# Kernel optimization log

Measured on AMD Instinct MI355X. Metric: run time of the kernel, lower is better.

Reference implementation:

```python
import jax, jax.numpy as jnp
import numpy as np


def _segsum(v, idx, n):
    return jax.ops.segment_sum(v, idx, num_segments=n)


def _rdl(z, n_dst, Wna, We, Wi, es, ed, is_, id_):
    """Relationship_Decoupled_layer: node softmax attn + per-edge attn.
    e-channel (mode etype): softmax over 2 logits; i-channel: sigmoid(1 logit)."""
    zd = z[:n_dst]
    node_alpha = jax.nn.softmax(zd @ Wna, axis=1)                      # [nd,2]
    e_e = jax.nn.softmax(jnp.concatenate([z[es], zd[ed]], axis=-1) @ We, axis=1)  # [Ee,2]
    e_i = jax.nn.sigmoid(jnp.concatenate([z[is_], zd[id_]], axis=-1) @ Wi)        # [Ei,1]
    return node_alpha, e_e, e_i


def _one_agg(z, n_dst, W, b, na, e_e, es, ed):
    """One_Neighbor_Aggregation: mean over nbrs of e[:,0]*Linear(z_src), relu, + alpha0*z_dst.
    Linear is applied on src nodes once (linearity) instead of per-edge."""
    zd = na[:, 0:1] * z[:n_dst]
    wz = z @ W + b                                                     # [n_src,D]
    s = _segsum(e_e[:, 0:1] * wz[es], ed, n_dst)                       # [nd,D]
    deg = _segsum(jnp.ones((es.shape[0], 1), z.dtype), ed, n_dst)
    f = jax.nn.relu(s / jnp.maximum(deg, 1.0))
    return f + zd


def _nia(z, n_dst, na, e_e, es, ed, e_i, is_, id_):
    """Neighbor_Interaction_Aggregation: e_h (mode etype, attn col 1) and i_h
    (other etype, sigmoid attn), cross term via polarization identity, + alpha1*z_dst."""
    zd = na[:, 1:2] * z[:n_dst]
    e_h = _segsum(e_e[:, 1:2] * z[es], ed, n_dst)
    i_h = _segsum(e_i * z[is_], id_, n_dst)
    inter = jax.nn.relu(0.5 * (jnp.square(e_h + i_h) - jnp.square(e_h) - jnp.square(i_h)))
    return inter + zd


def setup_inputs() -> dict:
    key = jax.random.key(0)
    ks = jax.random.split(key, 32)
    F, D, O = 256, 128, 64
    n_src0, n_dst0, E0 = 100000, 25000, 500000
    n_src1, n_dst1, E1 = 25000, 5000, 100000

    def ri(k, n, hi):
        return jax.random.randint(k, (n,), 0, hi, dtype=jnp.int32)

    inp = {
        'feat': jax.random.normal(ks[0], (n_src0, F), jnp.float32),
        'src0_cor': ri(ks[1], E0, n_src0), 'dst0_cor': ri(ks[2], E0, n_dst0),
        'src0_sim': ri(ks[3], E0, n_src0), 'dst0_sim': ri(ks[4], E0, n_dst0),
        'src1_cor': ri(ks[5], E1, n_src1), 'dst1_cor': ri(ks[6], E1, n_dst1),
        'src1_sim': ri(ks[7], E1, n_src1), 'dst1_sim': ri(ks[8], E1, n_dst1),
        'n_dst0': n_dst0, 'n_dst1': n_dst1,
    }
    s = 0.05  # keep attention logits / activations in a sane range
    inp['Win'] = jax.random.normal(ks[9], (2, F, D)) * s
    inp['b_in'] = jnp.zeros((2, D), jnp.float32)
    inp['na1'] = jax.random.normal(ks[10], (2, D, 2)) * s
    inp['ea1'] = jax.random.normal(ks[11], (2, 2 * D, 2)) * s
    inp['ia1'] = jax.random.normal(ks[12], (2, 2 * D, 1)) * s
    inp['W1'] = jax.random.normal(ks[13], (2, D, D)) * s
    inp['b1'] = jnp.zeros((2, D), jnp.float32)
    inp['na2'] = jax.random.normal(ks[14], (2, D, 2)) * s
    inp['ea2'] = jax.random.normal(ks[15], (2, 2 * D, 2)) * s
    inp['ia2'] = jax.random.normal(ks[16], (2, 2 * D, 1)) * s
    inp['W2'] = jax.random.normal(ks[17], (2, D, D)) * s
    inp['b2'] = jnp.zeros((2, D), jnp.float32)
    inp['Wout'] = jax.random.normal(ks[18], (2, D, O)) * s
    inp['bout'] = jnp.zeros((2, O), jnp.float32)
    return inp


def reference(feat, src0_cor, dst0_cor, src0_sim, dst0_sim,
              src1_cor, dst1_cor, src1_sim, dst1_sim, n_dst0, n_dst1,
              Win, b_in, na1, ea1, ia1, W1, b1, na2, ea2, ia2, W2, b2, Wout, bout):
    # mode index 0 = 'cor', 1 = 'sim'; e-channel = mode etype, i-channel = other etype
    blk0 = {0: (src0_cor, dst0_cor, src0_sim, dst0_sim),
            1: (src0_sim, dst0_sim, src0_cor, dst0_cor)}
    blk1 = {0: (src1_cor, dst1_cor, src1_sim, dst1_sim),
            1: (src1_sim, dst1_sim, src1_cor, dst1_cor)}
    outs = []
    for m in range(2):
        es0, ed0, is0, id0 = blk0[m]
        es1, ed1, is1, id1 = blk1[m]
        z = feat @ Win[m] + b_in[m]                                    # fc_input (eval: dropout = identity)
        # layer 1 on block0
        na, ee, ei = _rdl(z, n_dst0, na1[m], ea1[m], ia1[m], es0, ed0, is0, id0)
        one = _one_agg(z, n_dst0, W1[m], b1[m], na, ee, es0, ed0)
        nia = _nia(z, n_dst0, na, ee, es0, ed0, ei, is0, id0)
        z = 0.5 * (one + nia)                                          # [n_dst0, D]
        # layer 2 on block1
        na, ee, ei = _rdl(z, n_dst1, na2[m], ea2[m], ia2[m], es1, ed1, is1, id1)
        one = _one_agg(z, n_dst1, W2[m], b2[m], na, ee, es1, ed1)
        nia = _nia(z, n_dst1, na, ee, es1, ed1, ei, is1, id1)
        z = 0.5 * (one + nia)                                          # [n_dst1, D]
        outs.append(z @ Wout[m] + bout[m])
    return jnp.stack(outs)                                             # [2, n_dst1, O] (cor, sim)
```

## Files before the change

kernel.cpp:

```cpp
#include <hip/hip_runtime.h>
#include <hip/hip_bf16.h>
#include <math.h>

#define F_DIM 256
#define D_DIM 128
#define O_DIM 64
#define NS0   100000
#define ND0   25000
#define E0_N  500000
#define NS1   25000
#define ND1   5000
#define E1_N  100000

#define NBE0  1954
#define NBE1  391
#define NB_CSR (2 * NBE0 + 2 * NBE1)
#define NB_WPREP 576

typedef __attribute__((ext_vector_type(8))) short s8v;
typedef __attribute__((ext_vector_type(4))) float f4v;

struct CPtr4 { const int *p0, *p1, *p2, *p3; };
struct MPtr4 { int *p0, *p1, *p2, *p3; };

__device__ __forceinline__ float2 unpack2(uint u) {
    union { uint i; float f; } a, b;
    a.i = (u & 0xffffu) << 16; b.i = u & 0xffff0000u;
    return make_float2(a.f, b.f);
}
__device__ __forceinline__ ushort f2bf(float f) {
    __hip_bfloat16 h = __float2bfloat16(f);
    return *(ushort*)&h;
}
__device__ __forceinline__ float u2f(uint u) {
    union { uint i; float f; } v; v.i = u; return v.f;
}
__device__ __forceinline__ uint f2u(float f) {
    union { uint i; float f; } v; v.f = f; return v.i;
}

__global__ __launch_bounds__(256) void gemm_l0(
    const float* __restrict__ A,
    const ushort* __restrict__ Btb,
    const float* __restrict__ biasb,
    ushort* __restrict__ Coutb, size_t coutstr, int M)
{
    constexpr int PA = 40;
    __shared__ ushort As[64 * PA];
    __shared__ ushort Bs[2][128 * PA];

    const int tid = threadIdx.x;
    const int row0 = blockIdx.x * 64;
    const int wave = tid >> 6, lane = tid & 63;
    const int l15 = lane & 15, l4 = lane >> 4;
    const int wm0 = (wave >> 1) * 32;
    const int wn0 = (wave & 1) * 64;

    f4v acc[2][2][4];
    #pragma unroll
    for (int m2 = 0; m2 < 2; ++m2)
        #pragma unroll
        for (int i = 0; i < 2; ++i)
            #pragma unroll
            for (int j = 0; j < 4; ++j)
                acc[m2][i][j] = (f4v)(0.0f);

    for (int kc = 0; kc < F_DIM; kc += 32) {
        __syncthreads();
        {
            int r = tid >> 2, g = (tid & 3) * 8;
            int gr = row0 + r;
            float4 v0 = make_float4(0.f, 0.f, 0.f, 0.f);
            float4 v1 = make_float4(0.f, 0.f, 0.f, 0.f);
            if (gr < M) {
                v0 = *(const float4*)(A + (size_t)gr * F_DIM + kc + g);
                v1 = *(const float4*)(A + (size_t)gr * F_DIM + kc + g + 4);
            }
            ushort4 o0, o1;
            o0.x = f2bf(v0.x); o0.y = f2bf(v0.y); o0.z = f2bf(v0.z); o0.w = f2bf(v0.w);
            o1.x = f2bf(v1.x); o1.y = f2bf(v1.y); o1.z = f2bf(v1.z); o1.w = f2bf(v1.w);
            *(ushort4*)(&As[r * PA + g]) = o0;
            *(ushort4*)(&As[r * PA + g + 4]) = o1;
        }
        #pragma unroll
        for (int m2 = 0; m2 < 2; ++m2)
            #pragma unroll
            for (int it = 0; it < 2; ++it) {
                int f = tid + it * 256;
                int r = f >> 2, g = (f & 3) * 8;
                *(float4*)(&Bs[m2][r * PA + g]) =
                    *(const float4*)(Btb + m2 * (D_DIM * F_DIM) + (size_t)r * F_DIM + kc + g);
            }
        __syncthreads();

        s8v af[2];
        #pragma unroll
        for (int i = 0; i < 2; ++i)
            af[i] = *(const s8v*)(&As[(wm0 + i * 16 + l15) * PA + l4 * 8]);
        #pragma unroll
        for (int m2 = 0; m2 < 2; ++m2) {
            s8v bfr[4];
            #pragma unroll
            for (int j = 0; j < 4; ++j)
                bfr[j] = *(const s8v*)(&Bs[m2][(wn0 + j * 16 + l15) * PA + l4 * 8]);
            #pragma unroll
            for (int i = 0; i < 2; ++i)
                #pragma unroll
                for (int j = 0; j < 4; ++j)
                    acc[m2][i][j] = __builtin_amdgcn_mfma_f32_16x16x32_bf16(
                        af[i], bfr[j], acc[m2][i][j], 0, 0, 0);
        }
    }

    #pragma unroll
    for (int m2 = 0; m2 < 2; ++m2)
        #pragma unroll
        for (int i = 0; i < 2; ++i)
            #pragma unroll
            for (int ii = 0; ii < 4; ++ii) {
                int row = row0 + wm0 + i * 16 + l4 * 4 + ii;
                if (row < M) {
                    #pragma unroll
                    for (int j = 0; j < 4; ++j) {
                        int col = wn0 + j * 16 + l15;
                        Coutb[m2 * coutstr + (size_t)row * D_DIM + col] =
                            f2bf(acc[m2][i][j][ii] + biasb[m2 * D_DIM + col]);
                    }
                }
            }
}

template<int NW, int KD, int EPI>
__global__ __launch_bounds__(256) void mfma_gemm(
    const ushort* __restrict__ Ab, size_t astr,
    const ushort* __restrict__ Btb, size_t btstr,
    const float* __restrict__ biasb, size_t bstr,
    const float* __restrict__ cvecb, size_t cvstr,
    const float* __restrict__ partialb, size_t pstr,
    void* __restrict__ Coutb, size_t coutstr, int M)
{
    const int m = blockIdx.y;
    const ushort* A = Ab + m * astr;
    const ushort* Bt = Btb + m * btstr;
    const float* bias = biasb + m * bstr;
    const float* cvec = (EPI == 2) ? cvecb + m * cvstr : nullptr;
    const float* partial = (EPI == 2) ? partialb + m * pstr : nullptr;
    char* Cout = (char*)Coutb + m * coutstr * (EPI == 1 ? 4 : 2);

    constexpr int PA = 40;
    constexpr int WAVES_M = (NW == 128) ? 2 : 4;
    constexpr int WM = 128 / WAVES_M;
    constexpr int TM = WM / 16;
    constexpr int TN = 4;
    __shared__ ushort As[128 * PA];
    __shared__ ushort Bs[NW * PA];

    const int tid  = threadIdx.x;
    const int row0 = blockIdx.x * 128;
    const int wave = tid >> 6, lane = tid & 63;
    const int l15 = lane & 15, l4 = lane >> 4;
    int wm0, wn0;
    if (NW == 128) { wm0 = (wave >> 1) * 64; wn0 = (wave & 1) * 64; }
    else           { wm0 = wave * WM;        wn0 = 0; }

    f4v acc[TM][TN];
    #pragma unroll
    for (int i = 0; i < TM; ++i)
        #pragma unroll
        for (int j = 0; j < TN; ++j)
            acc[i][j] = (f4v)(0.0f);

    for (int kc = 0; kc < KD; kc += 32) {
        __syncthreads();
        #pragma unroll
        for (int it = 0; it < 2; ++it) {
            int f = tid + it * 256;
            int r = f >> 2, g = (f & 3) * 8;
            int gr = row0 + r;
            float4 v = make_float4(0.f, 0.f, 0.f, 0.f);
            if (gr < M) v = *(const float4*)(A + (size_t)gr * KD + kc + g);
            *(float4*)(&As[r * PA + g]) = v;
        }
        #pragma unroll
        for (int it = 0; it < NW * 32 / (256 * 8); ++it) {
            int f = tid + it * 256;
            int r = f >> 2, g = (f & 3) * 8;
            *(float4*)(&Bs[r * PA + g]) = *(const float4*)(Bt + (size_t)r * KD + kc + g);
        }
        __syncthreads();

        s8v af[TM], bfr[TN];
        #pragma unroll
        for (int i = 0; i < TM; ++i)
            af[i] = *(const s8v*)(&As[(wm0 + i * 16 + l15) * PA + l4 * 8]);
        #pragma unroll
        for (int j = 0; j < TN; ++j)
            bfr[j] = *(const s8v*)(&Bs[(wn0 + j * 16 + l15) * PA + l4 * 8]);
        #pragma unroll
        for (int i = 0; i < TM; ++i)
            #pragma unroll
            for (int j = 0; j < TN; ++j)
                acc[i][j] = __builtin_amdgcn_mfma_f32_16x16x32_bf16(
                    af[i], bfr[j], acc[i][j], 0, 0, 0);
    }

    #pragma unroll
    for (int i = 0; i < TM; ++i) {
        #pragma unroll
        for (int ii = 0; ii < 4; ++ii) {
            int row = row0 + wm0 + i * 16 + l4 * 4 + ii;
            if (row < M) {
                #pragma unroll
                for (int j = 0; j < TN; ++j) {
                    int col = wn0 + j * 16 + l15;
                    float a = acc[i][j][ii];
                    if (EPI == 1) {
                        ((float*)Cout)[(size_t)row * NW + col] = a + bias[col];
                    } else {
                        float val = a + cvec[row] * bias[col];
                        float o = partial[(size_t)row * NW + col] + 0.5f * fmaxf(val, 0.f);
                        ((ushort*)Cout)[(size_t)row * NW + col] = f2bf(o);
                    }
                }
            }
        }
    }
}

__global__ void histo4_prep(CPtr4 ed, MPtr4 cnt,
    const float* __restrict__ Win, const float* __restrict__ W1,
    const float* __restrict__ W2,  const float* __restrict__ Wout,
    ushort* __restrict__ Wtin, ushort* __restrict__ Wt1,
    ushort* __restrict__ Wt2,  ushort* __restrict__ Wtout)
{
    int b = blockIdx.x, t = threadIdx.x;
    if (b >= NB_CSR) {
        int i = (b - NB_CSR) * 256 + t;
        if (i < 65536) {
            int m = i >> 15, r = i & 32767, k = r >> 7, n = r & 127;
            Wtin[m * 32768 + n * 256 + k] = f2bf(Win[m * 32768 + k * 128 + n]);
        } else if (i < 98304) {
            int i2 = i - 65536;
            int m = i2 >> 14, r = i2 & 16383, k = r >> 7, n = r & 127;
            Wt1[m * 16384 + n * 128 + k] = f2bf(W1[m * 16384 + k * 128 + n]);
        } else if (i < 131072) {
            int i2 = i - 98304;
            int m = i2 >> 14, r = i2 & 16383, k = r >> 7, n = r & 127;
            Wt2[m * 16384 + n * 128 + k] = f2bf(W2[m * 16384 + k * 128 + n]);
        } else if (i < 147456) {
            int i2 = i - 131072;
            int m = i2 >> 13, r = i2 & 8191, k = r >> 6, n = r & 63;
            Wtout[m * 8192 + n * 128 + k] = f2bf(Wout[m * 8192 + k * 64 + n]);
        }
        return;
    }
    const int* edp; int* cp; int e, E;
    if (b < NBE0)          { edp = ed.p0; cp = cnt.p0; e = b * 256 + t;              E = E0_N; }
    else if (b < 2 * NBE0) { edp = ed.p1; cp = cnt.p1; e = (b - NBE0) * 256 + t;     E = E0_N; }
    else if (b < 2 * NBE0 + NBE1)
                           { edp = ed.p2; cp = cnt.p2; e = (b - 2 * NBE0) * 256 + t; E = E1_N; }
    else                   { edp = ed.p3; cp = cnt.p3; e = (b - 2 * NBE0 - NBE1) * 256 + t; E = E1_N; }
    if (e < E) atomicAdd(&cp[edp[e]], 1);
}

__global__ __launch_bounds__(1024) void exscan4(MPtr4 cnt, MPtr4 row, MPtr4 head)
{
    __shared__ int part[1024];
    const int b = blockIdx.x, t = threadIdx.x;
    int* cp; int* rp; int* hp; int n;
    if (b == 0)      { cp = cnt.p0; rp = row.p0; hp = head.p0; n = ND0; }
    else if (b == 1) { cp = cnt.p1; rp = row.p1; hp = head.p1; n = ND0; }
    else if (b == 2) { cp = cnt.p2; rp = row.p2; hp = head.p2; n = ND1; }
    else             { cp = cnt.p3; rp = row.p3; hp = head.p3; n = ND1; }

    const int chunk = (n + 1023) >> 10;
    const int start = t * chunk;
    int s = 0;
    for (int i = 0; i < chunk; ++i) {
        int idx = start + i;
        if (idx < n) s += cp[idx];
    }
    part[t] = s;
    __syncthreads();
    for (int off = 1; off < 1024; off <<= 1) {
        int v = (t >= off) ? part[t - off] : 0;
        __syncthreads();
        part[t] += v;
        __syncthreads();
    }
    int run = (t == 0) ? 0 : part[t - 1];
    for (int i = 0; i < chunk; ++i) {
        int idx = start + i;
        if (idx < n) { rp[idx] = run; hp[idx] = run; run += cp[idx]; }
    }
    if (t == 1023) rp[n] = part[1023];
}

__global__ void build4(CPtr4 es, CPtr4 ed, MPtr4 head, MPtr4 src)
{
    int b = blockIdx.x, t = threadIdx.x;
    const int *esp, *edp; int *hp, *sp; int e, E;
    if (b < NBE0)          { esp = es.p0; edp = ed.p0; hp = head.p0; sp = src.p0; e = b * 256 + t;              E = E0_N; }
    else if (b < 2 * NBE0) { esp = es.p1; edp = ed.p1; hp = head.p1; sp = src.p1; e = (b - NBE0) * 256 + t;     E = E0_N; }
    else if (b < 2 * NBE0 + NBE1)
                           { esp = es.p2; edp = ed.p2; hp = head.p2; sp = src.p2; e = (b - 2 * NBE0) * 256 + t; E = E1_N; }
    else                   { esp = es.p3; edp = ed.p3; hp = head.p3; sp = src.p3; e = (b - 2 * NBE0 - NBE1) * 256 + t; E = E1_N; }
    if (e >= E) return;
    int p = atomicAdd(&hp[edp[e]], 1);
    sp[p] = esp[e];
}

#define NP_NPB 128
__global__ __launch_bounds__(256) void node_proj(
    const ushort* __restrict__ zb, size_t zstr,
    const float* __restrict__ Web, const float* __restrict__ Wib,
    float* __restrict__ psb, float* __restrict__ qsb,
    float* __restrict__ pdb, float* __restrict__ qdb,
    int n_src, int n_dst)
{
    const int m = blockIdx.y;
    const ushort* z = zb + m * zstr;
    const float* We = Web + m * 512;
    const float* Wi = Wib + m * 256;
    float* ps = psb + (size_t)m * NS0 * 2;
    float* qs = qsb + (size_t)m * NS0;
    float* pd = pdb + (size_t)m * ND0 * 2;
    float* qd = qdb + (size_t)m * ND0;

    __shared__ float w[6][D_DIM];
    for (int k = threadIdx.x; k < D_DIM; k += 256) {
        w[0][k] = We[k * 2 + 0];
        w[1][k] = We[k * 2 + 1];
        w[2][k] = Wi[k];
        w[3][k] = We[(D_DIM + k) * 2 + 0];
        w[4][k] = We[(D_DIM + k) * 2 + 1];
        w[5][k] = Wi[D_DIM + k];
    }
    __syncthreads();

    const int sub = threadIdx.x & 7;
    const int g   = threadIdx.x >> 3;

    float wr[6][16];
    #pragma unroll
    for (int c = 0; c < 6; ++c)
        #pragma unroll
        for (int q = 0; q < 4; ++q) {
            float4 f = *(const float4*)(&w[c][sub * 16 + q * 4]);
            wr[c][q * 4 + 0] = f.x; wr[c][q * 4 + 1] = f.y;
            wr[c][q * 4 + 2] = f.z; wr[c][q * 4 + 3] = f.w;
        }

    #pragma unroll
    for (int it = 0; it < 4; ++it) {
        int node = blockIdx.x * NP_NPB + it * 32 + g;
        if (node >= n_src) continue;
        const ushort* zp = z + (size_t)node * D_DIM + sub * 16;
        uint4 ra = *(const uint4*)zp;
        uint4 rb = *(const uint4*)(zp + 8);
        uint rr[8] = {ra.x, ra.y, ra.z, ra.w, rb.x, rb.y, rb.z, rb.w};
        float p[6] = {0.f, 0.f, 0.f, 0.f, 0.f, 0.f};
        #pragma unroll
        for (int e = 0; e < 8; ++e) {
            float2 f2 = unpack2(rr[e]);
            #pragma unroll
            for (int c = 0; c < 6; ++c)
                p[c] += f2.x * wr[c][2 * e] + f2.y * wr[c][2 * e + 1];
        }
        #pragma unroll
        for (int off = 4; off > 0; off >>= 1)
            #pragma unroll
            for (int c = 0; c < 6; ++c)
                p[c] += __shfl_down(p[c], off);

        if (sub == 0) {
            *(float2*)(ps + (size_t)node * 2) = make_float2(p[0], p[1]);
            qs[node] = p[2];
            if (node < n_dst) {
                *(float2*)(pd + (size_t)node * 2) = make_float2(p[3], p[4]);
                qd[node] = p[5];
            }
        }
    }
}

__global__ __launch_bounds__(256) void edge_att(
    const float* __restrict__ psb, const float* __restrict__ pdb,
    const float* __restrict__ qsb, const float* __restrict__ qdb,
    const int* __restrict__ row_c, const int* __restrict__ src_c,
    const int* __restrict__ row_s, const int* __restrict__ src_s,
    uint2* __restrict__ epkb, uint2* __restrict__ ipkb,
    float* __restrict__ cvecb, int n_dst)
{
    const int m = blockIdx.y;
    const int d = blockIdx.x * 4 + (threadIdx.x >> 6);
    const int lane = threadIdx.x & 63;
    if (d >= n_dst) return;

    const float* ps = psb + (size_t)m * NS0 * 2;
    const float* qs = qsb + (size_t)m * NS0;
    const float* pdv = pdb + (size_t)m * ND0 * 2;
    const float* qdv = qdb + (size_t)m * ND0;
    const int* erow = m ? row_s : row_c;
    const int* esrc = m ? src_s : src_c;
    const int* irow = m ? row_c : row_s;
    const int* isrc = m ? src_c : src_s;
    uint2* epk = epkb + (size_t)m * E0_N;
    uint2* ipk = ipkb + (size_t)m * E0_N;
    float* cvec = cvecb + (size_t)m * ND0;

    const float pd0 = pdv[2 * d], pd1 = pdv[2 * d + 1];
    const float qdd = qdv[d];

    const int b0 = erow[d], b1 = erow[d + 1];
    float se0 = 0.f;
    for (int j = b0 + lane; j < b1; j += 64) {
        int s = esrc[j];
        float2 pp = *(const float2*)(ps + 2 * (size_t)s);
        float l0 = pp.x + pd0, l1 = pp.y + pd1;
        float mx = fmaxf(l0, l1);
        float x0 = __expf(l0 - mx), x1 = __expf(l1 - mx);
        float e0 = x0 / (x0 + x1);
        epk[j] = make_uint2(f2u(e0), (uint)s);
        se0 += e0;
    }
    #pragma unroll
    for (int off = 32; off > 0; off >>= 1)
        se0 += __shfl_down(se0, off);
    if (lane == 0) cvec[d] = se0 / fmaxf((float)(b1 - b0), 1.0f);

    const int c0 = irow[d], c1 = irow[d + 1];
    for (int j = c0 + lane; j < c1; j += 64) {
        int s = isrc[j];
        float q = qs[s] + qdd;
        float sg = 1.0f / (1.0f + __expf(-q));
        ipk[j] = make_uint2(f2u(sg), (uint)s);
    }
}

__global__ __launch_bounds__(256) void gather_acc(
    const ushort* __restrict__ zb, size_t zstr,
    const uint2* __restrict__ epkb, const uint2* __restrict__ ipkb,
    const int* __restrict__ row_c, const int* __restrict__ row_s,
    ushort* __restrict__ h0base, float* __restrict__ partialb, int n_dst)
{
    const int m = blockIdx.y;
    const int d = blockIdx.x * 4 + (threadIdx.x >> 6);
    const int lane = threadIdx.x & 63;
    if (d >= n_dst) return;

    const ushort* z = zb + m * zstr;
    const uint2* epk = epkb + (size_t)m * E0_N;
    const uint2* ipk = ipkb + (size_t)m * E0_N;
    const int* erow = m ? row_s : row_c;
    const int* irow = m ? row_c : row_s;
    ushort* h0b = h0base + (size_t)m * ND0 * D_DIM;
    float* partial = partialb + (size_t)m * ND0 * D_DIM;

    float h0x = 0.f, h0y = 0.f, szx = 0.f, szy = 0.f;
    float ihx = 0.f, ihy = 0.f;

    const int b0 = erow[d], b1 = erow[d + 1];
    int j = b0;
    const int jfull = b0 + ((b1 - b0) & ~7);
    for (; j < jfull; j += 8) {
        uint2 ew[8]; uint rr[8];
        #pragma unroll
        for (int k = 0; k < 8; ++k) ew[k] = epk[j + k];
        #pragma unroll
        for (int k = 0; k < 8; ++k) rr[k] = *(const uint*)(z + (size_t)ew[k].y * D_DIM + lane * 2);
        #pragma unroll
        for (int k = 0; k < 8; ++k) {
            float w0 = u2f(ew[k].x);
            float2 v = unpack2(rr[k]);
            szx += v.x; szy += v.y;
            h0x += w0 * v.x; h0y += w0 * v.y;
        }
    }
    if (j < b1) {
        uint2 ew[8]; uint rr[8];
        #pragma unroll
        for (int k = 0; k < 8; ++k) ew[k] = epk[j + k];
        #pragma unroll
        for (int k = 0; k < 8; ++k) {
            uint s = (j + k < b1) ? ew[k].y : 0u;
            rr[k] = *(const uint*)(z + (size_t)s * D_DIM + lane * 2);
        }
        #pragma unroll
        for (int k = 0; k < 8; ++k) {
            float sel = (j + k < b1) ? 1.0f : 0.0f;
            float w0 = u2f(ew[k].x) * sel;
            float2 v = unpack2(rr[k]);
            szx += v.x * sel; szy += v.y * sel;
            h0x += w0 * v.x; h0y += w0 * v.y;
        }
    }

    const int c0 = irow[d], c1 = irow[d + 1];
    j = c0;
    const int cfull = c0 + ((c1 - c0) & ~7);
    for (; j < cfull; j += 8) {
        uint2 ew[8]; uint rr[8];
        #pragma unroll
        for (int k = 0; k < 8; ++k) ew[k] = ipk[j + k];
        #pragma unroll
        for (int k = 0; k < 8; ++k) rr[k] = *(const uint*)(z + (size_t)ew[k].y * D_DIM + lane * 2);
        #pragma unroll
        for (int k = 0; k < 8; ++k) {
            float g = u2f(ew[k].x);
            float2 v = unpack2(rr[k]);
            ihx += g * v.x; ihy += g * v.y;
        }
    }
    if (j < c1) {
        uint2 ew[8]; uint rr[8];
        #pragma unroll
        for (int k = 0; k < 8; ++k) ew[k] = ipk[j + k];
        #pragma unroll
        for (int k = 0; k < 8; ++k) {
            uint s = (j + k < c1) ? ew[k].y : 0u;
            rr[k] = *(const uint*)(z + (size_t)s * D_DIM + lane * 2);
        }
        #pragma unroll
        for (int k = 0; k < 8; ++k) {
            float sel = (j + k < c1) ? 1.0f : 0.0f;
            float g = u2f(ew[k].x) * sel;
            float2 v = unpack2(rr[k]);
            ihx += g * v.x; ihy += g * v.y;
        }
    }

    float ehx = szx - h0x, ehy = szy - h0y;
    float inv = 1.0f / fmaxf((float)(b1 - b0), 1.0f);
    uint hp = (uint)f2bf(h0x * inv) | ((uint)f2bf(h0y * inv) << 16);
    *(uint*)(h0b + (size_t)d * D_DIM + lane * 2) = hp;

    float2 zd = unpack2(*(const uint*)(z + (size_t)d * D_DIM + lane * 2));
    float px = 0.5f * (fmaxf(ehx * ihx, 0.f) + zd.x);
    float py = 0.5f * (fmaxf(ehy * ihy, 0.f) + zd.y);
    *(float2*)(partial + (size_t)d * D_DIM + lane * 2) = make_float2(px, py);
}

extern "C" void kernel_launch(void* const* d_in, const int* in_sizes, int n_in,
                              void* d_out, int out_size, void* d_ws, size_t ws_size,
                              hipStream_t stream)
{
    const float* feat = (const float*)d_in[0];
    const int* src0_cor = (const int*)d_in[1];
    const int* dst0_cor = (const int*)d_in[2];
    const int* src0_sim = (const int*)d_in[3];
    const int* dst0_sim = (const int*)d_in[4];
    const int* src1_cor = (const int*)d_in[5];
    const int* dst1_cor = (const int*)d_in[6];
    const int* src1_sim = (const int*)d_in[7];
    const int* dst1_sim = (const int*)d_in[8];
    const float* Win  = (const float*)d_in[11];
    const float* b_in = (const float*)d_in[12];
    const float* ea1  = (const float*)d_in[14];
    const float* ia1  = (const float*)d_in[15];
    const float* W1   = (const float*)d_in[16];
    const float* b1   = (const float*)d_in[17];
    const float* ea2  = (const float*)d_in[19];
    const float* ia2  = (const float*)d_in[20];
    const float* W2   = (const float*)d_in[21];
    const float* b2   = (const float*)d_in[22];
    const float* Wout = (const float*)d_in[23];
    const float* bout = (const float*)d_in[24];
    (void)in_sizes; (void)n_in; (void)out_size; (void)ws_size;

    char* wsb = (char*)d_ws;
    size_t off = 0;
    auto alloc_f = [&](size_t n) { float*  p = (float*) (wsb + off); off += n * 4; return p; };
    auto alloc_i = [&](size_t n) { int*    p = (int*)   (wsb + off); off += n * 4; return p; };
    auto alloc_h = [&](size_t n) { ushort* p = (ushort*)(wsb + off); off += ((n * 2 + 15) & ~15ull); return p; };
    auto alloc_u2 = [&](size_t n) { uint2* p = (uint2*)(wsb + off); off += n * 8; return p; };

    ushort* z0b   = alloc_h((size_t)2 * NS0 * D_DIM);
    ushort* z1b   = alloc_h((size_t)2 * NS1 * D_DIM);
    ushort* z2b   = alloc_h((size_t)2 * ND1 * D_DIM);
    ushort* h0b   = alloc_h((size_t)2 * ND0 * D_DIM);
    ushort* Wtin  = alloc_h((size_t)2 * D_DIM * F_DIM);
    ushort* Wt1   = alloc_h((size_t)2 * D_DIM * D_DIM);
    ushort* Wt2   = alloc_h((size_t)2 * D_DIM * D_DIM);
    ushort* Wtout = alloc_h((size_t)2 * O_DIM * D_DIM);

    float* ps      = alloc_f((size_t)2 * NS0 * 2);
    float* qs      = alloc_f((size_t)2 * NS0);
    float* pd      = alloc_f((size_t)2 * ND0 * 2);
    float* qd      = alloc_f((size_t)2 * ND0);
    float* cvec    = alloc_f((size_t)2 * ND0);
    float* partial = alloc_f((size_t)2 * ND0 * D_DIM);
    uint2* epk     = alloc_u2((size_t)2 * E0_N + 8);
    uint2* ipk     = alloc_u2((size_t)2 * E0_N + 8);

    int* src_c0 = alloc_i(E0_N); int* row_c0 = alloc_i(ND0 + 1);
    int* src_s0 = alloc_i(E0_N); int* row_s0 = alloc_i(ND0 + 1);
    int* src_c1 = alloc_i(E1_N); int* row_c1 = alloc_i(ND1 + 1);
    int* src_s1 = alloc_i(E1_N); int* row_s1 = alloc_i(ND1 + 1);
    int* cnt_all  = alloc_i(2 * ND0 + 2 * ND1);
    int* head_all = alloc_i(2 * ND0 + 2 * ND1);

    int* cnt_c0 = cnt_all;            int* head_c0 = head_all;
    int* cnt_s0 = cnt_all + ND0;      int* head_s0 = head_all + ND0;
    int* cnt_c1 = cnt_all + 2 * ND0;  int* head_c1 = head_all + 2 * ND0;
    int* cnt_s1 = cnt_c1 + ND1;       int* head_s1 = head_c1 + ND1;

    hipMemsetAsync(cnt_all, 0, (size_t)(2 * ND0 + 2 * ND1) * 4, stream);
    {
        CPtr4 edp  = {dst0_cor, dst0_sim, dst1_cor, dst1_sim};
        CPtr4 esp  = {src0_cor, src0_sim, src1_cor, src1_sim};
        MPtr4 cntp = {cnt_c0, cnt_s0, cnt_c1, cnt_s1};
        MPtr4 rowp = {row_c0, row_s0, row_c1, row_s1};
        MPtr4 hdp  = {head_c0, head_s0, head_c1, head_s1};
        MPtr4 srcp = {src_c0, src_s0, src_c1, src_s1};
        histo4_prep<<<NB_CSR + NB_WPREP, 256, 0, stream>>>(
            edp, cntp, Win, W1, W2, Wout, Wtin, Wt1, Wt2, Wtout);
        exscan4<<<4, 1024, 0, stream>>>(cntp, rowp, hdp);
        build4<<<NB_CSR, 256, 0, stream>>>(esp, edp, hdp, srcp);
    }

    const size_t Z0S = (size_t)NS0 * D_DIM, Z1S = (size_t)NS1 * D_DIM;
    const size_t Z2S = (size_t)ND1 * D_DIM, H0S = (size_t)ND0 * D_DIM;

    gemm_l0<<<(NS0 + 63) / 64, 256, 0, stream>>>(
        feat, Wtin, b_in, z0b, Z0S, NS0);

    node_proj<<<dim3((NS0 + NP_NPB - 1) / NP_NPB, 2), 256, 0, stream>>>(
        z0b, Z0S, ea1, ia1, ps, qs, pd, qd, NS0, ND0);
    edge_att<<<dim3((ND0 + 3) / 4, 2), 256, 0, stream>>>(
        ps, pd, qs, qd, row_c0, src_c0, row_s0, src_s0, epk, ipk, cvec, ND0);
    gather_acc<<<dim3((ND0 + 3) / 4, 2), 256, 0, stream>>>(
        z0b, Z0S, epk, ipk, row_c0, row_s0, h0b, partial, ND0);
    mfma_gemm<128, 128, 2><<<dim3((ND0 + 127) / 128, 2), 256, 0, stream>>>(
        h0b, H0S, Wt1, (size_t)D_DIM * D_DIM, b1, D_DIM,
        cvec, ND0, partial, H0S, z1b, Z1S, ND0);

    node_proj<<<dim3((NS1 + NP_NPB - 1) / NP_NPB, 2), 256, 0, stream>>>(
        z1b, Z1S, ea2, ia2, ps, qs, pd, qd, NS1, ND1);
    edge_att<<<dim3((ND1 + 3) / 4, 2), 256, 0, stream>>>(
        ps, pd, qs, qd, row_c1, src_c1, row_s1, src_s1, epk, ipk, cvec, ND1);
    gather_acc<<<dim3((ND1 + 3) / 4, 2), 256, 0, stream>>>(
        z1b, Z1S, epk, ipk, row_c1, row_s1, h0b, partial, ND1);
    mfma_gemm<128, 128, 2><<<dim3((ND1 + 127) / 128, 2), 256, 0, stream>>>(
        h0b, H0S, Wt2, (size_t)D_DIM * D_DIM, b2, D_DIM,
        cvec, ND0, partial, H0S, z2b, Z2S, ND1);

    mfma_gemm<64, 128, 1><<<dim3((ND1 + 127) / 128, 2), 256, 0, stream>>>(
        z2b, Z2S, Wtout, (size_t)O_DIM * D_DIM, bout, O_DIM,
        nullptr, 0, nullptr, 0, (float*)d_out, (size_t)ND1 * O_DIM, ND1);
}
```

Measured before the change: 559.5 us.

## Fuse edge attention and neighbor gather into one kernel via LDS staging

Merges the edge_att and gather_acc kernels so each wave computes attention weights for up to 64 edges, stages weight/source pairs in shared memory, and immediately gathers neighbor features from them. This removes the global epk/ipk intermediate buffers (write then reread of about 16 MB per layer) and one launch per layer. In exchange, the attention computation now sits serially before each gather chunk within a wave, which may reduce memory-level parallelism. The LDS handoff relies on wave-local s_waitcnt with no barrier.

New measurement: 549.6 us. About the same (-1.8%).

```diff
diff --git a/kernel.cpp b/kernel.cpp
--- a/kernel.cpp
+++ b/kernel.cpp
@@ -384,19 +384,24 @@
     }
 }
 
-__global__ __launch_bounds__(256) void edge_att(
+__global__ __launch_bounds__(256) void edge_gather(
+    const ushort* __restrict__ zb, size_t zstr,
     const float* __restrict__ psb, const float* __restrict__ pdb,
     const float* __restrict__ qsb, const float* __restrict__ qdb,
     const int* __restrict__ row_c, const int* __restrict__ src_c,
     const int* __restrict__ row_s, const int* __restrict__ src_s,
-    uint2* __restrict__ epkb, uint2* __restrict__ ipkb,
+    ushort* __restrict__ h0base, float* __restrict__ partialb,
     float* __restrict__ cvecb, int n_dst)
 {
+    __shared__ uint2 sc[4][64];
+
     const int m = blockIdx.y;
-    const int d = blockIdx.x * 4 + (threadIdx.x >> 6);
+    const int wv = threadIdx.x >> 6;
+    const int d = blockIdx.x * 4 + wv;
     const int lane = threadIdx.x & 63;
     if (d >= n_dst) return;
 
+    const ushort* z = zb + m * zstr;
     const float* ps = psb + (size_t)m * NS0 * 2;
     const float* qs = qsb + (size_t)m * NS0;
     const float* pdv = pdb + (size_t)m * ND0 * 2;
@@ -405,128 +410,113 @@
     const int* esrc = m ? src_s : src_c;
     const int* irow = m ? row_c : row_s;
     const int* isrc = m ? src_c : src_s;
-    uint2* epk = epkb + (size_t)m * E0_N;
-    uint2* ipk = ipkb + (size_t)m * E0_N;
+    ushort* h0b = h0base + (size_t)m * ND0 * D_DIM;
+    float* partial = partialb + (size_t)m * ND0 * D_DIM;
     float* cvec = cvecb + (size_t)m * ND0;
 
     const float pd0 = pdv[2 * d], pd1 = pdv[2 * d + 1];
     const float qdd = qdv[d];
 
+    float h0x = 0.f, h0y = 0.f, szx = 0.f, szy = 0.f;
+    float ihx = 0.f, ihy = 0.f;
+    float se0 = 0.f;
+
     const int b0 = erow[d], b1 = erow[d + 1];
-    float se0 = 0.f;
-    for (int j = b0 + lane; j < b1; j += 64) {
-        int s = esrc[j];
-        float2 pp = *(const float2*)(ps + 2 * (size_t)s);
-        float l0 = pp.x + pd0, l1 = pp.y + pd1;
-        float mx = fmaxf(l0, l1);
-        float x0 = __expf(l0 - mx), x1 = __expf(l1 - mx);
-        float e0 = x0 / (x0 + x1);
-        epk[j] = make_uint2(f2u(e0), (uint)s);
-        se0 += e0;
-    }
+    for (int base = b0; base < b1; base += 64) {
+        const int cnt = min(64, b1 - base);
+        if (lane < cnt) {
+            int s = esrc[base + lane];
+            float2 pp = *(const float2*)(ps + 2 * (size_t)s);
+            float l0 = pp.x + pd0, l1 = pp.y + pd1;
+            float mx = fmaxf(l0, l1);
+            float x0 = __expf(l0 - mx), x1 = __expf(l1 - mx);
+            float e0 = x0 / (x0 + x1);
+            sc[wv][lane] = make_uint2(f2u(e0), (uint)s);
+            se0 += e0;
+        }
+        asm volatile("s_waitcnt lgkmcnt(0)" ::: "memory");
+        const int kf = cnt & ~7;
+        int k = 0;
+        for (; k < kf; k += 8) {
+            uint2 ew[8]; uint rr[8];
+            #pragma unroll
+            for (int t = 0; t < 8; ++t) ew[t] = sc[wv][k + t];
+            #pragma unroll
+            for (int t = 0; t < 8; ++t) rr[t] = *(const uint*)(z + (size_t)ew[t].y * D_DIM + lane * 2);
+            #pragma unroll
+            for (int t = 0; t < 8; ++t) {
+                float w0 = u2f(ew[t].x);
+                float2 v = unpack2(rr[t]);
+                szx += v.x; szy += v.y;
+                h0x += w0 * v.x; h0y += w0 * v.y;
+            }
+        }
+        if (k < cnt) {
+            uint2 ew[8]; uint rr[8];
+            #pragma unroll
+            for (int t = 0; t < 8; ++t) ew[t] = sc[wv][(k + t) & 63];
+            #pragma unroll
+            for (int t = 0; t < 8; ++t) {
+                uint s = (k + t < cnt) ? ew[t].y : 0u;
+                rr[t] = *(const uint*)(z + (size_t)s * D_DIM + lane * 2);
+            }
+            #pragma unroll
+            for (int t = 0; t < 8; ++t) {
+                float sel = (k + t < cnt) ? 1.0f : 0.0f;
+                float w0 = u2f(ew[t].x) * sel;
+                float2 v = unpack2(rr[t]);
+                szx += v.x * sel; szy += v.y * sel;
+                h0x += w0 * v.x; h0y += w0 * v.y;
+            }
+        }
+    }
+
     #pragma unroll
     for (int off = 32; off > 0; off >>= 1)
         se0 += __shfl_down(se0, off);
     if (lane == 0) cvec[d] = se0 / fmaxf((float)(b1 - b0), 1.0f);
 
     const int c0 = irow[d], c1 = irow[d + 1];
-    for (int j = c0 + lane; j < c1; j += 64) {
-        int s = isrc[j];
-        float q = qs[s] + qdd;
-        float sg = 1.0f / (1.0f + __expf(-q));
-        ipk[j] = make_uint2(f2u(sg), (uint)s);
-    }
-}
-
-__global__ __launch_bounds__(256) void gather_acc(
-    const ushort* __restrict__ zb, size_t zstr,
-    const uint2* __restrict__ epkb, const uint2* __restrict__ ipkb,
-    const int* __restrict__ row_c, const int* __restrict__ row_s,
-    ushort* __restrict__ h0base, float* __restrict__ partialb, int n_dst)
-{
-    const int m = blockIdx.y;
-    const int d = blockIdx.x * 4 + (threadIdx.x >> 6);
-    const int lane = threadIdx.x & 63;
-    if (d >= n_dst) return;
-
-    const ushort* z = zb + m * zstr;
-    const uint2* epk = epkb + (size_t)m * E0_N;
-    const uint2* ipk = ipkb + (size_t)m * E0_N;
-    const int* erow = m ? row_s : row_c;
-    const int* irow = m ? row_c : row_s;
-    ushort* h0b = h0base + (size_t)m * ND0 * D_DIM;
-    float* partial = partialb + (size_t)m * ND0 * D_DIM;
-
-    float h0x = 0.f, h0y = 0.f, szx = 0.f, szy = 0.f;
-    float ihx = 0.f, ihy = 0.f;
-
-    const int b0 = erow[d], b1 = erow[d + 1];
-    int j = b0;
-    const int jfull = b0 + ((b1 - b0) & ~7);
-    for (; j < jfull; j += 8) {
-        uint2 ew[8]; uint rr[8];
-        #pragma unroll
-        for (int k = 0; k < 8; ++k) ew[k] = epk[j + k];
-        #pragma unroll
-        for (int k = 0; k < 8; ++k) rr[k] = *(const uint*)(z + (size_t)ew[k].y * D_DIM + lane * 2);
-        #pragma unroll
-        for (int k = 0; k < 8; ++k) {
-            float w0 = u2f(ew[k].x);
-            float2 v = unpack2(rr[k]);
-            szx += v.x; szy += v.y;
-            h0x += w0 * v.x; h0y += w0 * v.y;
-        }
-    }
-    if (j < b1) {
-        uint2 ew[8]; uint rr[8];
-        #pragma unroll
-        for (int k = 0; k < 8; ++k) ew[k] = epk[j + k];
-        #pragma unroll
-        for (int k = 0; k < 8; ++k) {
-            uint s = (j + k < b1) ? ew[k].y : 0u;
-            rr[k] = *(const uint*)(z + (size_t)s * D_DIM + lane * 2);
-        }
-        #pragma unroll
-        for (int k = 0; k < 8; ++k) {
-            float sel = (j + k < b1) ? 1.0f : 0.0f;
-            float w0 = u2f(ew[k].x) * sel;
-            float2 v = unpack2(rr[k]);
-            szx += v.x * sel; szy += v.y * sel;
-            h0x += w0 * v.x; h0y += w0 * v.y;
-        }
-    }
-
-    const int c0 = irow[d], c1 = irow[d + 1];
-    j = c0;
-    const int cfull = c0 + ((c1 - c0) & ~7);
-    for (; j < cfull; j += 8) {
-        uint2 ew[8]; uint rr[8];
-        #pragma unroll
-        for (int k = 0; k < 8; ++k) ew[k] = ipk[j + k];
-        #pragma unroll
-        for (int k = 0; k < 8; ++k) rr[k] = *(const uint*)(z + (size_t)ew[k].y * D_DIM + lane * 2);
-        #pragma unroll
-        for (int k = 0; k < 8; ++k) {
-            float g = u2f(ew[k].x);
-            float2 v = unpack2(rr[k]);
-            ihx += g * v.x; ihy += g * v.y;
-        }
-    }
-    if (j < c1) {
-        uint2 ew[8]; uint rr[8];
-        #pragma unroll
-        for (int k = 0; k < 8; ++k) ew[k] = ipk[j + k];
-        #pragma unroll
-        for (int k = 0; k < 8; ++k) {
-            uint s = (j + k < c1) ? ew[k].y : 0u;
-            rr[k] = *(const uint*)(z + (size_t)s * D_DIM + lane * 2);
-        }
-        #pragma unroll
-        for (int k = 0; k < 8; ++k) {
-            float sel = (j + k < c1) ? 1.0f : 0.0f;
-            float g = u2f(ew[k].x) * sel;
-            float2 v = unpack2(rr[k]);
-            ihx += g * v.x; ihy += g * v.y;
+    for (int base = c0; base < c1; base += 64) {
+        const int cnt = min(64, c1 - base);
+        if (lane < cnt) {
+            int s = isrc[base + lane];
+            float q = qs[s] + qdd;
+            float sg = 1.0f / (1.0f + __expf(-q));
+            sc[wv][lane] = make_uint2(f2u(sg), (uint)s);
+        }
+        asm volatile("s_waitcnt lgkmcnt(0)" ::: "memory");
+        const int kf = cnt & ~7;
+        int k = 0;
+        for (; k < kf; k += 8) {
+            uint2 ew[8]; uint rr[8];
+            #pragma unroll
+            for (int t = 0; t < 8; ++t) ew[t] = sc[wv][k + t];
+            #pragma unroll
+            for (int t = 0; t < 8; ++t) rr[t] = *(const uint*)(z + (size_t)ew[t].y * D_DIM + lane * 2);
+            #pragma unroll
+            for (int t = 0; t < 8; ++t) {
+                float g = u2f(ew[t].x);
+                float2 v = unpack2(rr[t]);
+                ihx += g * v.x; ihy += g * v.y;
+            }
+        }
+        if (k < cnt) {
+            uint2 ew[8]; uint rr[8];
+            #pragma unroll
+            for (int t = 0; t < 8; ++t) ew[t] = sc[wv][(k + t) & 63];
+            #pragma unroll
+            for (int t = 0; t < 8; ++t) {
+                uint s = (k + t < cnt) ? ew[t].y : 0u;
+                rr[t] = *(const uint*)(z + (size_t)s * D_DIM + lane * 2);
+            }
+            #pragma unroll
+            for (int t = 0; t < 8; ++t) {
+                float sel = (k + t < cnt) ? 1.0f : 0.0f;
+                float g = u2f(ew[t].x) * sel;
+                float2 v = unpack2(rr[t]);
+                ihx += g * v.x; ihy += g * v.y;
+            }
         }
     }
 
@@ -573,7 +563,6 @@
     auto alloc_f = [&](size_t n) { float*  p = (float*) (wsb + off); off += n * 4; return p; };
     auto alloc_i = [&](size_t n) { int*    p = (int*)   (wsb + off); off += n * 4; return p; };
     auto alloc_h = [&](size_t n) { ushort* p = (ushort*)(wsb + off); off += ((n * 2 + 15) & ~15ull); return p; };
-    auto alloc_u2 = [&](size_t n) { uint2* p = (uint2*)(wsb + off); off += n * 8; return p; };
 
     ushort* z0b   = alloc_h((size_t)2 * NS0 * D_DIM);
     ushort* z1b   = alloc_h((size_t)2 * NS1 * D_DIM);
@@ -590,8 +579,6 @@
     float* qd      = alloc_f((size_t)2 * ND0);
     float* cvec    = alloc_f((size_t)2 * ND0);
     float* partial = alloc_f((size_t)2 * ND0 * D_DIM);
-    uint2* epk     = alloc_u2((size_t)2 * E0_N + 8);
-    uint2* ipk     = alloc_u2((size_t)2 * E0_N + 8);
 
     int* src_c0 = alloc_i(E0_N); int* row_c0 = alloc_i(ND0 + 1);
     int* src_s0 = alloc_i(E0_N); int* row_s0 = alloc_i(ND0 + 1);
@@ -627,20 +614,18 @@
 
     node_proj<<<dim3((NS0 + NP_NPB - 1) / NP_NPB, 2), 256, 0, stream>>>(
         z0b, Z0S, ea1, ia1, ps, qs, pd, qd, NS0, ND0);
-    edge_att<<<dim3((ND0 + 3) / 4, 2), 256, 0, stream>>>(
-        ps, pd, qs, qd, row_c0, src_c0, row_s0, src_s0, epk, ipk, cvec, ND0);
-    gather_acc<<<dim3((ND0 + 3) / 4, 2), 256, 0, stream>>>(
-        z0b, Z0S, epk, ipk, row_c0, row_s0, h0b, partial, ND0);
+    edge_gather<<<dim3((ND0 + 3) / 4, 2), 256, 0, stream>>>(
+        z0b, Z0S, ps, pd, qs, qd, row_c0, src_c0, row_s0, src_s0,
+        h0b, partial, cvec, ND0);
     mfma_gemm<128, 128, 2><<<dim3((ND0 + 127) / 128, 2), 256, 0, stream>>>(
         h0b, H0S, Wt1, (size_t)D_DIM * D_DIM, b1, D_DIM,
         cvec, ND0, partial, H0S, z1b, Z1S, ND0);
 
     node_proj<<<dim3((NS1 + NP_NPB - 1) / NP_NPB, 2), 256, 0, stream>>>(
         z1b, Z1S, ea2, ia2, ps, qs, pd, qd, NS1, ND1);
-    edge_att<<<dim3((ND1 + 3) / 4, 2), 256, 0, stream>>>(
-        ps, pd, qs, qd, row_c1, src_c1, row_s1, src_s1, epk, ipk, cvec, ND1);
-    gather_acc<<<dim3((ND1 + 3) / 4, 2), 256, 0, stream>>>(
-        z1b, Z1S, epk, ipk, row_c1, row_s1, h0b, partial, ND1);
+    edge_gather<<<dim3((ND1 + 3) / 4, 2), 256, 0, stream>>>(
+        z1b, Z1S, ps, pd, qs, qd, row_c1, src_c1, row_s1, src_s1,
+        h0b, partial, cvec, ND1);
     mfma_gemm<128, 128, 2><<<dim3((ND1 + 127) / 128, 2), 256, 0, stream>>>(
         h0b, H0S, Wt2, (size_t)D_DIM * D_DIM, b2, D_DIM,
         cvec, ND0, partial, H0S, z2b, Z2S, ND1);
```
